# Kernel optimization log

Hardware: AMD Instinct MI355X
Metric: run time of the kernel (lower is better)

The kernel has to match this reference:

```python
import jax, jax.numpy as jnp
import numpy as np
import math

B, N, D, K = 8, 2048, 1024, 128
PI = math.pi


def setup_inputs() -> dict:
    key = jax.random.key(0)
    ks = jax.random.split(key, 4)
    x = jax.random.normal(ks[0], (B, N, D), dtype=jnp.float32)
    W_proj = jax.random.normal(ks[1], (D, 6 * K), dtype=jnp.float32) * (D ** -0.5)
    # structured bias init as in OscillatorProjection._init_weights
    b = np.zeros(6 * K, np.float32)
    groups = [K // 4, K // 2, K - K // 4 - K // 2]
    centers = [0.3, 0.65, 0.97]
    off = 3 * K
    for n_k, c in zip(groups, centers):
        b[off:off + n_k] = math.log(c / (1.0 - c))
        off += n_k
    b[4 * K:5 * K] = math.log(0.65 / 0.35)
    b[5 * K:] = -2.0
    b_proj = jnp.asarray(b)
    omega_base = jnp.exp(jnp.linspace(math.log(2.0 * PI / N), math.log(PI * (1.0 - 1.0 / K)), K)).astype(jnp.float32)
    W_phase = jax.random.normal(ks[2], (D, K), dtype=jnp.float32) * 0.001
    b_phase = jnp.zeros((K,), jnp.float32)
    W_res = jax.random.normal(ks[3], (4 * K - 2, D), dtype=jnp.float32) * 0.002
    lambda_pcg = jnp.float32(0.5)
    res_scale = jnp.float32(0.05)
    return dict(x=x, W_proj=W_proj, b_proj=b_proj, omega_base=omega_base,
                W_phase=W_phase, b_phase=b_phase, W_res=W_res,
                lambda_pcg=lambda_pcg, res_scale=res_scale)


def _resonance_scan(alpha, drive):
    # linear recurrence r_t = alpha_t * r_{t-1} + d_t, r_0 = 0, along axis=1
    def combine(e1, e2):
        a1, b1 = e1
        a2, b2 = e2
        return (a2 * a1, a2 * b1 + b2)
    _, r = jax.lax.associative_scan(combine, (alpha, drive), axis=1)
    return r


def reference(x, W_proj, b_proj, omega_base, W_phase, b_phase, W_res, lambda_pcg, res_scale):
    _, n, _ = x.shape
    out = x @ W_proj + b_proj  # [B, n, 6K]
    A_r, Om_r, Ph_r, Ga_r, Go_r, Be_r = jnp.split(out, 6, axis=-1)
    A = jnp.minimum(jax.nn.softplus(A_r), 3.0)
    omega = jnp.clip(jax.nn.sigmoid(Om_r) * PI + omega_base, 1e-4, PI - 1e-4)
    phi = jnp.tanh(Ph_r) * PI
    alpha = jax.nn.sigmoid(Ga_r)
    g_out = jax.nn.sigmoid(Go_r)
    beta = jax.nn.sigmoid(Be_r)
    positions = jnp.log1p(jnp.arange(n, dtype=jnp.float32)).reshape(1, n, 1)
    angle = omega * positions + phi
    cos_a = jnp.cos(angle)
    sin_a = jnp.sin(angle)
    drive = (1.0 - alpha) * A
    # fused real/imag scan sharing alpha (mirrors the fused Triton path)
    r = _resonance_scan(jnp.concatenate([alpha, alpha], axis=-1),
                        jnp.concatenate([drive * cos_a, drive * sin_a], axis=-1))
    r_r, r_i = r[..., :K], r[..., K:]
    readout = r_r * cos_a + r_i * sin_a
    r_r = r_r - beta * readout * cos_a
    r_i = r_i - beta * readout * sin_a
    # state norm: rescale only when |r| > 1
    modulus = jnp.sqrt(r_r ** 2 + r_i ** 2 + 1e-8)
    scale = jnp.maximum(modulus, 1.0)
    r_r = r_r / scale
    r_i = r_i / scale
    # rotate into the oscillator frame
    rho_re = r_r * cos_a + r_i * sin_a
    rho_im = -r_r * sin_a + r_i * cos_a
    rho_norm = jnp.sqrt(rho_re ** 2 + rho_im ** 2 + 1e-6)
    pq = x @ W_phase + b_phase
    align = (rho_re * jnp.cos(pq) + rho_im * jnp.sin(pq)) / rho_norm
    gate = jax.nn.sigmoid(lambda_pcg * align)
    rho_re = gate * rho_re
    rho_im = gate * rho_im
    # SCPM: adjacent-oscillator complex cross products -> 4K-2 features
    cross_re = rho_re[..., :-1] * rho_re[..., 1:] + rho_im[..., :-1] * rho_im[..., 1:]
    cross_im = rho_im[..., :-1] * rho_re[..., 1:] - rho_re[..., :-1] * rho_im[..., 1:]
    feats = jnp.concatenate([g_out * rho_re, g_out * rho_im, cross_re, cross_im], axis=-1)
    return x + res_scale * (feats @ W_res)
```

## Files before the change

kernel.cpp:

```cpp
#include <hip/hip_runtime.h>
#include <math.h>

#define PI_F 3.14159265358979323846f
#define SEG 128
#define SLEN 16
typedef unsigned short u16;
typedef __attribute__((ext_vector_type(8))) short bf16x8;
typedef __attribute__((ext_vector_type(4))) float f32x4;

__device__ __forceinline__ float sigmoidf_(float x){ return __fdividef(1.0f, 1.0f+__expf(-x)); }
__device__ __forceinline__ float softplusf_(float x){
    return fmaxf(x, 0.f) + __logf(1.f + __expf(-fabsf(x)));
}
__device__ __forceinline__ float tanhpi_(float x){
    float t = __expf(-2.f*fabsf(x));
    float th = __fdividef(1.f - t, 1.f + t);
    return copysignf(th, x)*PI_F;
}
__device__ __forceinline__ void fsincos(float a, float* s, float* c){
    float r = a * 0.15915494309189535f;
    r = r - floorf(r);
#if __has_builtin(__builtin_amdgcn_sinf)
    *s = __builtin_amdgcn_sinf(r);
    *c = __builtin_amdgcn_cosf(r);
#else
    float t = r * 6.283185307179586f;
    *s = __sinf(t); *c = __cosf(t);
#endif
}
__device__ __forceinline__ u16 f2bf(float f){
    unsigned u = __float_as_uint(f);
    return (u16)((u + 0x7FFFu + ((u>>16)&1u)) >> 16);
}
__device__ __forceinline__ float b2f(u16 v){
    return __uint_as_float(((unsigned)v)<<16);
}
__device__ __forceinline__ void gl_lds16(const u16* g, u16* l){
    __builtin_amdgcn_global_load_lds((const __attribute__((address_space(1))) void*)g,
                                     (__attribute__((address_space(3))) void*)l, 16, 0, 0);
}

__global__ __launch_bounds__(256) void k_cvt_x(const float* __restrict__ x, u16* __restrict__ xb){
    size_t i = ((size_t)blockIdx.x*256 + threadIdx.x)*8;
    float4 v0 = *(const float4*)&x[i];
    float4 v1 = *(const float4*)&x[i+4];
    ushort4 a = make_ushort4(f2bf(v0.x),f2bf(v0.y),f2bf(v0.z),f2bf(v0.w));
    ushort4 b = make_ushort4(f2bf(v1.x),f2bf(v1.y),f2bf(v1.z),f2bf(v1.w));
    *(ushort4*)&xb[i]   = a;
    *(ushort4*)&xb[i+4] = b;
}

__global__ __launch_bounds__(256) void k_tcvt(const float* __restrict__ W, u16* __restrict__ Wt,
                                              int K, int Ns, int KD){
    __shared__ float s[32][33];
    const int tx = threadIdx.x & 31, ty = threadIdx.x >> 5;
    const int k0 = blockIdx.y*32, n0 = blockIdx.x*32;
    #pragma unroll
    for (int i=0;i<4;i++){
        int k = k0 + ty + i*8;
        s[ty+i*8][tx] = (k < K) ? W[(size_t)k*Ns + n0 + tx] : 0.f;
    }
    __syncthreads();
    #pragma unroll
    for (int i=0;i<4;i++){
        int n = n0 + ty + i*8;
        Wt[(size_t)n*KD + k0 + tx] = f2bf(s[tx][ty+i*8]);
    }
}

__global__ __launch_bounds__(256) void k_mm1(
    const u16* __restrict__ A,
    const u16* __restrict__ Bt,
    const float* __restrict__ bp, const float* __restrict__ bph,
    u16* __restrict__ C)
{
    const int bid = blockIdx.x;
    const int swz = (bid & 7)*112 + (bid >> 3);
    const int by = swz / 7, bx = swz - by*7;

    __shared__ u16 As[128*32];
    __shared__ u16 Bs[128*32];
    const int tid = threadIdx.x;
    const int w = tid>>6, lane = tid&63;
    const int wm = w>>1, wn = w&1;
    const int r0 = by*128, c0 = bx*128;

    const u16* ga[2]; const u16* gb[2]; u16 *la[2], *lb[2];
    #pragma unroll
    for (int i=0;i<2;i++){
        ga[i] = A  + (size_t)(r0 + w*32 + i*16 + (lane>>2))*1024 + (lane&3)*8;
        gb[i] = Bt + (size_t)(c0 + w*32 + i*16 + (lane>>2))*1024 + (lane&3)*8;
        la[i] = As + w*1024 + i*512;
        lb[i] = Bs + w*1024 + i*512;
    }
    const int lr = lane&15, lk = lane>>4;
    const int ao = (wm*64 + lr)*32 + lk*8;
    const int bo = (wn*64 + lr)*32 + lk*8;

    f32x4 acc[4][4] = {};
    for (int k0=0; k0<1024; k0+=32){
        gl_lds16(ga[0]+k0, la[0]); gl_lds16(ga[1]+k0, la[1]);
        gl_lds16(gb[0]+k0, lb[0]); gl_lds16(gb[1]+k0, lb[1]);
        __syncthreads();
        bf16x8 af[4], bfr[4];
        #pragma unroll
        for (int m=0;m<4;m++) af[m]  = *(const bf16x8*)&As[ao + m*512];
        #pragma unroll
        for (int n=0;n<4;n++) bfr[n] = *(const bf16x8*)&Bs[bo + n*512];
        #pragma unroll
        for (int m=0;m<4;m++)
            #pragma unroll
            for (int n=0;n<4;n++)
                acc[m][n] = __builtin_amdgcn_mfma_f32_16x16x32_bf16(af[m], bfr[n], acc[m][n], 0,0,0);
        __syncthreads();
    }
    #pragma unroll
    for (int n=0;n<4;n++){
        int col = c0 + wn*64 + n*16 + lr;
        float bl = (col < 768) ? bp[col] : bph[col-768];
        #pragma unroll
        for (int m=0;m<4;m++){
            int row = r0 + wm*64 + m*16 + lk*4;
            #pragma unroll
            for (int r=0;r<4;r++)
                C[(size_t)(row+r)*896 + col] = f2bf(acc[m][n][r] + bl);
        }
    }
}

__global__ __launch_bounds__(256) void k_mm2(
    const u16* __restrict__ A,
    const u16* __restrict__ Bt,
    const u16* __restrict__ Xb,
    const float* __restrict__ rs_p,
    float* __restrict__ O)
{
    const int bid = blockIdx.x;
    const int swz = (bid & 7)*128 + (bid >> 3);
    const int by = swz >> 3, bx = swz & 7;

    __shared__ u16 As[128*32];
    __shared__ u16 Bs[128*32];
    const int tid = threadIdx.x;
    const int w = tid>>6, lane = tid&63;
    const int wm = w>>1, wn = w&1;
    const int r0 = by*128, c0 = bx*128;

    const u16* ga[2]; const u16* gb[2]; u16 *la[2], *lb[2];
    #pragma unroll
    for (int i=0;i<2;i++){
        ga[i] = A  + (size_t)(r0 + w*32 + i*16 + (lane>>2))*512 + (lane&3)*8;
        gb[i] = Bt + (size_t)(c0 + w*32 + i*16 + (lane>>2))*512 + (lane&3)*8;
        la[i] = As + w*1024 + i*512;
        lb[i] = Bs + w*1024 + i*512;
    }
    const int lr = lane&15, lk = lane>>4;
    const int ao = (wm*64 + lr)*32 + lk*8;
    const int bo = (wn*64 + lr)*32 + lk*8;

    f32x4 acc[4][4] = {};
    for (int k0=0; k0<512; k0+=32){
        gl_lds16(ga[0]+k0, la[0]); gl_lds16(ga[1]+k0, la[1]);
        gl_lds16(gb[0]+k0, lb[0]); gl_lds16(gb[1]+k0, lb[1]);
        __syncthreads();
        bf16x8 af[4], bfr[4];
        #pragma unroll
        for (int m=0;m<4;m++) af[m]  = *(const bf16x8*)&As[ao + m*512];
        #pragma unroll
        for (int n=0;n<4;n++) bfr[n] = *(const bf16x8*)&Bs[bo + n*512];
        #pragma unroll
        for (int m=0;m<4;m++)
            #pragma unroll
            for (int n=0;n<4;n++)
                acc[m][n] = __builtin_amdgcn_mfma_f32_16x16x32_bf16(af[m], bfr[n], acc[m][n], 0,0,0);
        __syncthreads();
    }
    const float rs = rs_p[0];
    #pragma unroll
    for (int n=0;n<4;n++){
        int col = c0 + wn*64 + n*16 + lr;
        #pragma unroll
        for (int m=0;m<4;m++){
            int row = r0 + wm*64 + m*16 + lk*4;
            #pragma unroll
            for (int r=0;r<4;r++){
                size_t idx = (size_t)(row+r)*1024 + col;
                O[idx] = b2f(Xb[idx]) + rs*acc[m][n][r];
            }
        }
    }
}

__global__ __launch_bounds__(128) void k_s1(
    const u16* __restrict__ C1,
    const float* __restrict__ omega_base,
    float* __restrict__ Ag, float* __restrict__ Br, float* __restrict__ Bi)
{
    const int k = threadIdx.x;
    const int seg = blockIdx.x, b = blockIdx.y;
    const float ob = omega_base[k];
    const int n0 = seg*SLEN;
    float aag = 1.f, br = 0.f, bi = 0.f;
    #pragma unroll 4
    for (int s=0; s<SLEN; s++){
        const int n = n0 + s;
        const u16* row = C1 + (size_t)(b*2048+n)*896;
        float Ar = b2f(row[k]);
        float Om = b2f(row[128+k]);
        float Ph = b2f(row[256+k]);
        float Ga = b2f(row[384+k]);
        float alpha = sigmoidf_(Ga);
        float A = fminf(softplusf_(Ar), 3.0f);
        float omega = fminf(fmaxf(sigmoidf_(Om)*PI_F + ob, 1e-4f), PI_F-1e-4f);
        float phi = tanhpi_(Ph);
        float pos = __logf(1.f + (float)n);
        float sa, ca; fsincos(fmaf(omega, pos, phi), &sa, &ca);
        float drive = (1.f-alpha)*A;
        aag *= alpha;
        br = fmaf(alpha, br, drive*ca);
        bi = fmaf(alpha, bi, drive*sa);
    }
    const size_t o = (size_t)(b*SEG + seg)*128 + k;
    Ag[o] = aag; Br[o] = br; Bi[o] = bi;
}

__global__ __launch_bounds__(256) void k_s2(
    const float* __restrict__ Ag, const float* __restrict__ Br, const float* __restrict__ Bi,
    float* __restrict__ Pr, float* __restrict__ Pi)
{
    const int gid = blockIdx.x*256 + threadIdx.x;
    const int b = gid >> 7, k = gid & 127;
    float pr = 0.f, pi = 0.f;
    #pragma unroll 8
    for (int seg=0; seg<SEG; seg++){
        const size_t o = (size_t)(b*SEG + seg)*128 + k;
        float a = Ag[o], r = Br[o], i = Bi[o];
        Pr[o] = pr; Pi[o] = pi;
        pr = fmaf(a, pr, r);
        pi = fmaf(a, pi, i);
    }
}

__global__ __launch_bounds__(128) void k_s3(
    const u16* __restrict__ C1,
    const float* __restrict__ omega_base,
    const float* __restrict__ lam_p,
    const float* __restrict__ Pr, const float* __restrict__ Pi,
    u16* __restrict__ F)
{
    const int k = threadIdx.x;
    const int seg = blockIdx.x, b = blockIdx.y;
    const float ob = omega_base[k];
    const float lam = lam_p[0];
    __shared__ float sre[2][129], sim[2][129];

    const size_t po = (size_t)(b*SEG + seg)*128 + k;
    float rr = Pr[po], ri = Pi[po];
    const int n0 = seg*SLEN;

    #pragma unroll 2
    for (int s=0; s<SLEN; s++){
        const int n = n0 + s;
        const u16* row = C1 + (size_t)(b*2048+n)*896;
        float Ar = b2f(row[k]);
        float Om = b2f(row[128+k]);
        float Ph = b2f(row[256+k]);
        float Ga = b2f(row[384+k]);
        float Go = b2f(row[512+k]);
        float Be = b2f(row[640+k]);
        float pq = b2f(row[768+k]);
        float alpha = sigmoidf_(Ga);
        float A = fminf(softplusf_(Ar), 3.0f);
        float omega = fminf(fmaxf(sigmoidf_(Om)*PI_F + ob, 1e-4f), PI_F-1e-4f);
        float phi = tanhpi_(Ph);
        float pos = __logf(1.f + (float)n);
        float sa, ca; fsincos(fmaf(omega, pos, phi), &sa, &ca);
        float drive = (1.f-alpha)*A;
        rr = fmaf(alpha, rr, drive*ca);
        ri = fmaf(alpha, ri, drive*sa);
        float readout = rr*ca + ri*sa;
        float beta = sigmoidf_(Be);
        float r2r = rr - beta*readout*ca;
        float r2i = ri - beta*readout*sa;
        float m2 = r2r*r2r + r2i*r2i + 1e-8f;
        float inv = fminf(rsqrtf(m2), 1.0f);
        r2r *= inv; r2i *= inv;
        float rho_re =  r2r*ca + r2i*sa;
        float rho_im = -r2r*sa + r2i*ca;
        float rho2 = rho_re*rho_re + rho_im*rho_im + 1e-6f;
        float spq, cpq; fsincos(pq, &spq, &cpq);
        float align = (rho_re*cpq + rho_im*spq)*rsqrtf(rho2);
        float gate = sigmoidf_(lam*align);
        rho_re *= gate; rho_im *= gate;
        float go = sigmoidf_(Go);

        const int buf = s & 1;
        sre[buf][k] = rho_re; sim[buf][k] = rho_im;
        __syncthreads();

        u16* frow = F + (size_t)(b*2048+n)*512;
        frow[k]       = f2bf(go*rho_re);
        frow[128 + k] = f2bf(go*rho_im);
        if (k < 127){
            float nre = sre[buf][k+1], nim = sim[buf][k+1];
            frow[256 + k] = f2bf(rho_re*nre + rho_im*nim);
            frow[383 + k] = f2bf(rho_im*nre - rho_re*nim);
        } else {
            frow[510] = 0; frow[511] = 0;
        }
    }
}

extern "C" void kernel_launch(void* const* d_in, const int* in_sizes, int n_in,
                              void* d_out, int out_size, void* d_ws, size_t ws_size,
                              hipStream_t stream)
{
    const float* x   = (const float*)d_in[0];
    const float* Wp  = (const float*)d_in[1];
    const float* bp  = (const float*)d_in[2];
    const float* ob  = (const float*)d_in[3];
    const float* Wph = (const float*)d_in[4];
    const float* bph = (const float*)d_in[5];
    const float* Wr  = (const float*)d_in[6];
    const float* lam = (const float*)d_in[7];
    const float* rs  = (const float*)d_in[8];
    float* out = (float*)d_out;

    char* ws = (char*)d_ws;
    u16*   C1  = (u16*)  (ws + 0);
    float* Ag  = (float*)(ws + 29360128);
    float* Brr = (float*)(ws + 29884416);
    float* Bii = (float*)(ws + 30408704);
    float* Pr  = (float*)(ws + 30932992);
    float* Pi  = (float*)(ws + 31457280);
    u16*   F   = (u16*)  (ws + 31981568);
    u16*   Xb  = (u16*)  (ws + 58720256);
    u16*   Wt  = (u16*)  (ws + 92274688);
    u16*   Wrt = (u16*)  (ws + 94109696);

    dim3 blk(256);
    hipLaunchKernelGGL(k_cvt_x, dim3(8192),   blk, 0, stream, x, Xb);
    hipLaunchKernelGGL(k_tcvt,  dim3(24,32),  blk, 0, stream, Wp,  Wt,            1024, 768,  1024);
    hipLaunchKernelGGL(k_tcvt,  dim3(4,32),   blk, 0, stream, Wph, Wt + 768*1024, 1024, 128,  1024);
    hipLaunchKernelGGL(k_tcvt,  dim3(32,16),  blk, 0, stream, Wr,  Wrt,           510,  1024, 512);
    hipLaunchKernelGGL(k_mm1,   dim3(896),    blk, 0, stream, Xb, Wt, bp, bph, C1);
    hipLaunchKernelGGL(k_s1,    dim3(SEG,8),  dim3(128), 0, stream, C1, ob, Ag, Brr, Bii);
    hipLaunchKernelGGL(k_s2,    dim3(4),      blk, 0, stream, Ag, Brr, Bii, Pr, Pi);
    hipLaunchKernelGGL(k_s3,    dim3(SEG,8),  dim3(128), 0, stream, C1, ob, lam, Pr, Pi, F);
    hipLaunchKernelGGL(k_mm2,   dim3(1024),   blk, 0, stream, F, Wrt, Xb, rs, out);
}
```

Baseline: 148.1 us.

## Rewrite projection GEMM with 256x256 tiles and triple-buffered LDS pipeline

Measured after the change: 143.8 us. 2.9% less time.

```diff
diff --git a/kernel.cpp b/kernel.cpp
--- a/kernel.cpp
+++ b/kernel.cpp
@@ -68,62 +68,109 @@
     }
 }
 
-__global__ __launch_bounds__(256) void k_mm1(
+__global__ __launch_bounds__(512,1) void k_mm1(
     const u16* __restrict__ A,
     const u16* __restrict__ Bt,
     const float* __restrict__ bp, const float* __restrict__ bph,
     u16* __restrict__ C)
 {
+    __shared__ u16 sm[3*16384];
     const int bid = blockIdx.x;
-    const int swz = (bid & 7)*112 + (bid >> 3);
-    const int by = swz / 7, bx = swz - by*7;
-
-    __shared__ u16 As[128*32];
-    __shared__ u16 Bs[128*32];
+    const int swz = (bid & 7)*32 + (bid >> 3);
+    const int by = swz >> 2, bx = swz & 3;
+    const int r0 = by*256, c0 = bx*256;
     const int tid = threadIdx.x;
-    const int w = tid>>6, lane = tid&63;
-    const int wm = w>>1, wn = w&1;
-    const int r0 = by*128, c0 = bx*128;
-
-    const u16* ga[2]; const u16* gb[2]; u16 *la[2], *lb[2];
-    #pragma unroll
-    for (int i=0;i<2;i++){
-        ga[i] = A  + (size_t)(r0 + w*32 + i*16 + (lane>>2))*1024 + (lane&3)*8;
-        gb[i] = Bt + (size_t)(c0 + w*32 + i*16 + (lane>>2))*1024 + (lane&3)*8;
-        la[i] = As + w*1024 + i*512;
-        lb[i] = Bs + w*1024 + i*512;
-    }
-    const int lr = lane&15, lk = lane>>4;
-    const int ao = (wm*64 + lr)*32 + lk*8;
-    const int bo = (wn*64 + lr)*32 + lk*8;
-
-    f32x4 acc[4][4] = {};
-    for (int k0=0; k0<1024; k0+=32){
-        gl_lds16(ga[0]+k0, la[0]); gl_lds16(ga[1]+k0, la[1]);
-        gl_lds16(gb[0]+k0, lb[0]); gl_lds16(gb[1]+k0, lb[1]);
-        __syncthreads();
+    const int w = tid >> 6, lane = tid & 63;
+    const int wm = w >> 2, wn = w & 3;
+    const int lr = lane & 15, lk = lane >> 4;
+
+    const u16* gA = A  + (size_t)(r0 + w*32 + (lane>>2))*1024 + (lane&3)*8;
+    const u16* gB = Bt + (size_t)(c0 + w*32 + (lane>>2))*1024 + (lane&3)*8;
+    const int ldsA = w*1024;
+    const int ldsB = 8192 + w*1024;
+
+    const int aoff = (wm*128 + lr)*32 + lk*8;
+    const int boff = 8192 + (wn*64 + lr)*32 + lk*8;
+
+    f32x4 acc[8][4] = {};
+
+    #pragma unroll
+    for (int j=0;j<2;j++){
+        gl_lds16(gA + j*16*1024,      sm + ldsA + j*512);
+        gl_lds16(gB + j*16*1024,      sm + ldsB + j*512);
+    }
+    #pragma unroll
+    for (int j=0;j<2;j++){
+        gl_lds16(gA + j*16*1024 + 32, sm + 16384 + ldsA + j*512);
+        gl_lds16(gB + j*16*1024 + 32, sm + 16384 + ldsB + j*512);
+    }
+    asm volatile("s_waitcnt vmcnt(4)" ::: "memory");
+    __builtin_amdgcn_s_barrier();
+    __builtin_amdgcn_sched_barrier(0);
+
+    for (int k=0; k<32; ++k){
+        const u16* bufp = sm + (k%3)*16384;
+        u16*       bufn = sm + ((k+2)%3)*16384;
+        const int  k0n  = (k+2)*32;
         bf16x8 af[4], bfr[4];
-        #pragma unroll
-        for (int m=0;m<4;m++) af[m]  = *(const bf16x8*)&As[ao + m*512];
-        #pragma unroll
-        for (int n=0;n<4;n++) bfr[n] = *(const bf16x8*)&Bs[bo + n*512];
+
+        #pragma unroll
+        for (int m=0;m<4;m++) af[m]  = *(const bf16x8*)&bufp[aoff + m*512];
+        #pragma unroll
+        for (int n=0;n<4;n++) bfr[n] = *(const bf16x8*)&bufp[boff + n*512];
+        if (k < 30){
+            gl_lds16(gA + k0n,           bufn + ldsA);
+            gl_lds16(gA + 16*1024 + k0n, bufn + ldsA + 512);
+        }
+        __builtin_amdgcn_s_barrier();
+        __builtin_amdgcn_sched_barrier(0);
+        asm volatile("s_waitcnt lgkmcnt(0)" ::: "memory");
+        __builtin_amdgcn_sched_barrier(0);
+        __builtin_amdgcn_s_setprio(1);
         #pragma unroll
         for (int m=0;m<4;m++)
             #pragma unroll
             for (int n=0;n<4;n++)
-                acc[m][n] = __builtin_amdgcn_mfma_f32_16x16x32_bf16(af[m], bfr[n], acc[m][n], 0,0,0);
-        __syncthreads();
-    }
-    #pragma unroll
-    for (int n=0;n<4;n++){
-        int col = c0 + wn*64 + n*16 + lr;
-        float bl = (col < 768) ? bp[col] : bph[col-768];
-        #pragma unroll
-        for (int m=0;m<4;m++){
-            int row = r0 + wm*64 + m*16 + lk*4;
-            #pragma unroll
-            for (int r=0;r<4;r++)
-                C[(size_t)(row+r)*896 + col] = f2bf(acc[m][n][r] + bl);
+                acc[m][n] = __builtin_amdgcn_mfma_f32_16x16x32_bf16(af[m], bfr[n], acc[m][n],0,0,0);
+        __builtin_amdgcn_s_setprio(0);
+        __builtin_amdgcn_s_barrier();
+        __builtin_amdgcn_sched_barrier(0);
+
+        #pragma unroll
+        for (int m=0;m<4;m++) af[m] = *(const bf16x8*)&bufp[aoff + (m+4)*512];
+        if (k < 30){
+            gl_lds16(gB + k0n,           bufn + ldsB);
+            gl_lds16(gB + 16*1024 + k0n, bufn + ldsB + 512);
+        }
+        __builtin_amdgcn_s_barrier();
+        __builtin_amdgcn_sched_barrier(0);
+        asm volatile("s_waitcnt lgkmcnt(0)" ::: "memory");
+        __builtin_amdgcn_sched_barrier(0);
+        __builtin_amdgcn_s_setprio(1);
+        #pragma unroll
+        for (int m=0;m<4;m++)
+            #pragma unroll
+            for (int n=0;n<4;n++)
+                acc[m+4][n] = __builtin_amdgcn_mfma_f32_16x16x32_bf16(af[m], bfr[n], acc[m+4][n],0,0,0);
+        __builtin_amdgcn_s_setprio(0);
+        if (k < 30)       asm volatile("s_waitcnt vmcnt(4)" ::: "memory");
+        else if (k == 30) asm volatile("s_waitcnt vmcnt(0)" ::: "memory");
+        __builtin_amdgcn_s_barrier();
+        __builtin_amdgcn_sched_barrier(0);
+    }
+
+    if (c0 + wn*64 < 896){
+        #pragma unroll
+        for (int n=0;n<4;n++){
+            const int col = c0 + wn*64 + n*16 + lr;
+            const float bl = (col < 768) ? bp[col] : bph[col-768];
+            #pragma unroll
+            for (int m=0;m<8;m++){
+                const int row = r0 + wm*128 + m*16 + lk*4;
+                #pragma unroll
+                for (int r=0;r<4;r++)
+                    C[(size_t)(row+r)*896 + col] = f2bf(acc[m][n][r] + bl);
+            }
         }
     }
 }
@@ -334,16 +381,17 @@
     float* Pr  = (float*)(ws + 30932992);
     float* Pi  = (float*)(ws + 31457280);
     u16*   F   = (u16*)  (ws + 31981568);
+    u16*   Wt  = (u16*)  (ws + 48758784);
+    u16*   Wrt = (u16*)  (ws + 50855936);
     u16*   Xb  = (u16*)  (ws + 58720256);
-    u16*   Wt  = (u16*)  (ws + 92274688);
-    u16*   Wrt = (u16*)  (ws + 94109696);
 
     dim3 blk(256);
+    hipMemsetAsync(Wt, 0, 2097152, stream);
     hipLaunchKernelGGL(k_cvt_x, dim3(8192),   blk, 0, stream, x, Xb);
     hipLaunchKernelGGL(k_tcvt,  dim3(24,32),  blk, 0, stream, Wp,  Wt,            1024, 768,  1024);
     hipLaunchKernelGGL(k_tcvt,  dim3(4,32),   blk, 0, stream, Wph, Wt + 768*1024, 1024, 128,  1024);
     hipLaunchKernelGGL(k_tcvt,  dim3(32,16),  blk, 0, stream, Wr,  Wrt,           510,  1024, 512);
-    hipLaunchKernelGGL(k_mm1,   dim3(896),    blk, 0, stream, Xb, Wt, bp, bph, C1);
+    hipLaunchKernelGGL(k_mm1,   dim3(256),    dim3(512), 0, stream, Xb, Wt, bp, bph, C1);
     hipLaunchKernelGGL(k_s1,    dim3(SEG,8),  dim3(128), 0, stream, C1, ob, Ag, Brr, Bii);
     hipLaunchKernelGGL(k_s2,    dim3(4),      blk, 0, stream, Ag, Brr, Bii, Pr, Pi);
     hipLaunchKernelGGL(k_s3,    dim3(SEG,8),  dim3(128), 0, stream, C1, ob, lam, Pr, Pi, F);
```
